# Kernel tuning notes

Hardware: AMD Instinct MI355X
Metric: run time of the kernel (lower is better)

Reference implementation:

```python
import jax, jax.numpy as jnp
import numpy as np

N_NODES = 50000
N_EDGES = 1600000
D_IN = 512
D_HEAD = 64
N_HEADS_L1 = 4


def _segment_mean(data, seg_ids, num_segments, counts):
    s = jax.ops.segment_sum(data, seg_ids, num_segments=num_segments)
    denom = jnp.maximum(counts, 1.0)
    return jnp.where(counts[:, None] > 0, s / denom[:, None], 0.0)


def setup_inputs() -> dict:
    key = jax.random.key(0)
    k1, k2, k3, k4 = jax.random.split(key, 4)
    node_features = jax.random.normal(k1, (N_NODES, D_IN), dtype=jnp.float32)
    edge_index = jax.random.randint(k2, (2, N_EDGES), 0, N_NODES, dtype=jnp.int32)
    W1 = jax.random.normal(k3, (N_HEADS_L1, D_IN, D_HEAD), dtype=jnp.float32) * (1.0 / np.sqrt(D_IN))
    W2 = jax.random.normal(k4, (N_HEADS_L1 * D_HEAD, D_HEAD), dtype=jnp.float32) * (1.0 / np.sqrt(N_HEADS_L1 * D_HEAD))
    return {"node_features": node_features, "edge_index": edge_index, "W1": W1, "W2": W2}


def reference(node_features, edge_index, W1, W2):
    n = node_features.shape[0]
    src = edge_index[0]  # segment ids (destination of aggregation in TF code)
    dst = edge_index[1]  # gathered neighbors
    counts = jax.ops.segment_sum(jnp.ones_like(src, dtype=node_features.dtype), src, num_segments=n)

    # Layer 1: 4 heads, Dense(64, no bias) -> gather(dst) -> unsorted_segment_mean(src) -> concat -> elu
    head_outs = []
    for i in range(N_HEADS_L1):
        t = node_features @ W1[i]                 # (N, 64)
        agg = _segment_mean(t[dst], src, n, counts)  # (N, 64)
        head_outs.append(agg)
    h = jax.nn.elu(jnp.concatenate(head_outs, axis=-1))  # (N, 256)

    # Layer 2: 1 head, linear activation
    t2 = h @ W2                                   # (N, 64)
    out = _segment_mean(t2[dst], src, n, counts)  # (N, 64)
    return out
```

## Files before the change

kernel.cpp:

```cpp
#include <hip/hip_runtime.h>
#include <hip/hip_bf16.h>
#include <stdint.h>

#define N_NODES 50000
#define N_EDGES 1600000
#define D_IN    512
#define D_H1    256
#define D_OUT   64

#define NBUK    196
#define MAXB    9216
#define EPB     4096
#define NPB     391
#define SLOT    96

typedef __attribute__((ext_vector_type(8))) short  short8;
typedef __attribute__((ext_vector_type(4))) float  f32x4;
typedef __attribute__((ext_vector_type(4))) unsigned int u32x4;
typedef __attribute__((ext_vector_type(2))) unsigned int u32x2;

static __device__ __forceinline__ unsigned short f2bf(float f) {
    union { float f; unsigned int u; } c; c.f = f;
    unsigned int u = c.u;
    return (unsigned short)((u + 0x7FFFu + ((u >> 16) & 1u)) >> 16);
}
static __device__ __forceinline__ float bf2f(unsigned short b) {
    union { unsigned int u; float f; } c; c.u = ((unsigned int)b) << 16;
    return c.f;
}
static __device__ __forceinline__ float bflo(unsigned int v) { return bf2f((unsigned short)(v & 0xffffu)); }
static __device__ __forceinline__ float bfhi(unsigned int v) { return bf2f((unsigned short)(v >> 16)); }


__global__ __launch_bounds__(256) void part_kernel(const int* __restrict__ src,
                                                   const int* __restrict__ dst,
                                                   int* __restrict__ gcnt,
                                                   unsigned int* __restrict__ gbuk) {
    __shared__ int hist[NBUK];
    __shared__ int lofs[NBUK];
    __shared__ int gbase[NBUK];
    __shared__ int sbuf[256];
    __shared__ unsigned int sorted[EPB];
    __shared__ unsigned char bid[EPB];

    const int t  = threadIdx.x;
    const int e0 = blockIdx.x * EPB;
    int ec = N_EDGES - e0; if (ec > EPB) ec = EPB;

    for (int i = t; i < NBUK; i += 256) hist[i] = 0;
    __syncthreads();

    unsigned int rec[16];
    int bb[16], idx[16];
#pragma unroll
    for (int j = 0; j < 16; ++j) {
        int i = j * 256 + t;
        if (i < ec) {
            int s = src[e0 + i], d = dst[e0 + i];
            int b = s >> 8;
            rec[j] = ((unsigned int)(s & 255) << 16) | (unsigned int)d;
            bb[j]  = b;
            idx[j] = atomicAdd(&hist[b], 1);
        } else bb[j] = -1;
    }
    __syncthreads();

    int v = (t < NBUK) ? hist[t] : 0;
    sbuf[t] = v;
    __syncthreads();
#pragma unroll
    for (int off = 1; off < 256; off <<= 1) {
        int x = (t >= off) ? sbuf[t - off] : 0;
        __syncthreads();
        sbuf[t] += x;
        __syncthreads();
    }
    if (t < NBUK) {
        lofs[t]  = sbuf[t] - v;
        gbase[t] = atomicAdd(&gcnt[t], v);
    }
    __syncthreads();

#pragma unroll
    for (int j = 0; j < 16; ++j) {
        if (bb[j] >= 0) {
            int p = lofs[bb[j]] + idx[j];
            sorted[p] = rec[j];
            bid[p] = (unsigned char)bb[j];
        }
    }
    __syncthreads();

    for (int i = t; i < ec; i += 256) {
        int b = bid[i];
        int p = gbase[b] + (i - lofs[b]);
        gbuk[(size_t)b * MAXB + p] = sorted[i];
    }
}


__global__ __launch_bounds__(256) void sort_kernel(const int* __restrict__ gcnt,
                                                   const unsigned int* __restrict__ gbuk,
                                                   unsigned short* __restrict__ sdst,
                                                   int* __restrict__ deg) {
    __shared__ int hist[256];
    __shared__ int nofs[256];
    __shared__ int sbuf[256];
    __shared__ unsigned short list[MAXB];

    const int t = threadIdx.x;
    const int b = blockIdx.x;
    const int cnt = gcnt[b];
    const unsigned int* buk = gbuk + (size_t)b * MAXB;

    hist[t] = 0;
    __syncthreads();
    for (int i = t; i < cnt; i += 256)
        atomicAdd(&hist[buk[i] >> 16], 1);
    __syncthreads();

    int v = hist[t];
    sbuf[t] = v;
    __syncthreads();
#pragma unroll
    for (int off = 1; off < 256; off <<= 1) {
        int x = (t >= off) ? sbuf[t - off] : 0;
        __syncthreads();
        sbuf[t] += x;
        __syncthreads();
    }
    nofs[t] = sbuf[t] - v;
    const int n = b * 256 + t;
    if (n < N_NODES) deg[n] = v;
    __syncthreads();

    for (int i = t; i < cnt; i += 256) {
        unsigned int r = buk[i];
        int p = atomicAdd(&nofs[r >> 16], 1);
        list[p] = (unsigned short)(r & 0xffffu);
    }
    __syncthreads();

    if (n < N_NODES && v > 0) {
        int beg = nofs[t] - v;
        unsigned short* out = sdst + (size_t)n * SLOT;
        for (int j = 0; j < v; ++j) out[j] = list[beg + j];
    }
}


__global__ void convw_kernel(const float* __restrict__ W1, const float* __restrict__ W2,
                             unsigned short* __restrict__ Bt1, unsigned short* __restrict__ Bt2) {
    int i = blockIdx.x * 256 + threadIdx.x;
    if (i < 4 * 512 * 64) {
        int h = i >> 15;
        int k = (i >> 6) & 511;
        int j = i & 63;
        Bt1[(h * 64 + j) * 512 + k] = f2bf(W1[i]);
    } else {
        int r = i - 4 * 512 * 64;
        if (r < 256 * 64) {
            int k = r >> 6;
            int n = r & 63;
            Bt2[n * 256 + k] = f2bf(W2[r]);
        }
    }
}


__global__ __launch_bounds__(512) void gemm1_kernel(const float* __restrict__ A,
                                                    const unsigned short* __restrict__ Bt,
                                                    unsigned short* __restrict__ C) {
    constexpr int BM = 128, BN = 256, BK = 32, LDK = 40, K = D_IN, M = N_NODES, N = D_H1;
    __shared__ unsigned short As[BM * LDK];
    __shared__ unsigned short Bs[BN * LDK];

    const int tid  = threadIdx.x;
    const int lane = tid & 63;
    const int w    = tid >> 6;
    const int wm   = (w >> 2) * 64;
    const int wn   = (w & 3) * 64;
    const int quad = lane >> 4;
    const int l15  = lane & 15;
    const int bm   = blockIdx.x;

    f32x4 acc[4][4];
#pragma unroll
    for (int mi = 0; mi < 4; ++mi)
#pragma unroll
        for (int ni = 0; ni < 4; ++ni)
            acc[mi][ni] = (f32x4){0.f, 0.f, 0.f, 0.f};

    const int r0 = tid >> 2;
    const int f8 = tid & 3;

    for (int k0 = 0; k0 < K; k0 += BK) {
        {
            int grow = bm * BM + r0;
            if (grow >= M) grow = M - 1;
            const float* ap = A + (size_t)grow * K + k0 + f8 * 8;
            f32x4 v0 = *(const f32x4*)ap;
            f32x4 v1 = *(const f32x4*)(ap + 4);
            u32x4 pk;
            pk[0] = (unsigned int)f2bf(v0[0]) | ((unsigned int)f2bf(v0[1]) << 16);
            pk[1] = (unsigned int)f2bf(v0[2]) | ((unsigned int)f2bf(v0[3]) << 16);
            pk[2] = (unsigned int)f2bf(v1[0]) | ((unsigned int)f2bf(v1[1]) << 16);
            pk[3] = (unsigned int)f2bf(v1[2]) | ((unsigned int)f2bf(v1[3]) << 16);
            *(u32x4*)&As[r0 * LDK + f8 * 8] = pk;
        }
        {
#pragma unroll
            for (int p = 0; p < 2; ++p) {
                int row = p * 128 + r0;
                u32x4 v = *(const u32x4*)(Bt + (size_t)row * K + k0 + f8 * 8);
                *(u32x4*)&Bs[row * LDK + f8 * 8] = v;
            }
        }
        __syncthreads();

        short8 af[4], bfr[4];
#pragma unroll
        for (int mi = 0; mi < 4; ++mi)
            af[mi] = *(const short8*)&As[(wm + mi * 16 + l15) * LDK + quad * 8];
#pragma unroll
        for (int ni = 0; ni < 4; ++ni)
            bfr[ni] = *(const short8*)&Bs[(wn + ni * 16 + l15) * LDK + quad * 8];
#pragma unroll
        for (int mi = 0; mi < 4; ++mi)
#pragma unroll
            for (int ni = 0; ni < 4; ++ni)
                acc[mi][ni] = __builtin_amdgcn_mfma_f32_16x16x32_bf16(af[mi], bfr[ni], acc[mi][ni], 0, 0, 0);
        __syncthreads();
    }

#pragma unroll
    for (int mi = 0; mi < 4; ++mi) {
        int row0 = bm * BM + wm + mi * 16 + quad * 4;
#pragma unroll
        for (int ni = 0; ni < 4; ++ni) {
            int col = wn + ni * 16 + l15;
#pragma unroll
            for (int r = 0; r < 4; ++r) {
                int row = row0 + r;
                if (row < M) C[(size_t)row * N + col] = f2bf(acc[mi][ni][r]);
            }
        }
    }
}


__global__ __launch_bounds__(256) void gemm2_kernel(const unsigned short* __restrict__ A,
                                                    const unsigned short* __restrict__ Bt,
                                                    unsigned short* __restrict__ C) {
    constexpr int BM = 64, BN = 64, BK = 32, LDK = 40, K = D_H1, M = N_NODES, N = D_OUT;
    __shared__ unsigned short As[BM * LDK];
    __shared__ unsigned short Bs[BN * LDK];

    const int tid  = threadIdx.x;
    const int lane = tid & 63;
    const int w    = tid >> 6;
    const int wm   = (w >> 1) * 32;
    const int wn   = (w & 1) * 32;
    const int quad = lane >> 4;
    const int l15  = lane & 15;
    const int bm   = blockIdx.x;

    f32x4 acc[2][2];
#pragma unroll
    for (int mi = 0; mi < 2; ++mi)
#pragma unroll
        for (int ni = 0; ni < 2; ++ni)
            acc[mi][ni] = (f32x4){0.f, 0.f, 0.f, 0.f};

    for (int k0 = 0; k0 < K; k0 += BK) {
        {
            int f8 = tid & 3;
            int r0 = tid >> 2;
            int grow = bm * BM + r0;
            if (grow >= M) grow = M - 1;
            u32x4 v = *(const u32x4*)(A + (size_t)grow * K + k0 + f8 * 8);
            *(u32x4*)&As[r0 * LDK + f8 * 8] = v;
        }
        {
            int f8 = tid & 3;
            int r0 = tid >> 2;
            u32x4 v = *(const u32x4*)(Bt + (size_t)r0 * K + k0 + f8 * 8);
            *(u32x4*)&Bs[r0 * LDK + f8 * 8] = v;
        }
        __syncthreads();

        short8 af[2], bfr[2];
#pragma unroll
        for (int mi = 0; mi < 2; ++mi)
            af[mi] = *(const short8*)&As[(wm + mi * 16 + l15) * LDK + quad * 8];
#pragma unroll
        for (int ni = 0; ni < 2; ++ni)
            bfr[ni] = *(const short8*)&Bs[(wn + ni * 16 + l15) * LDK + quad * 8];
#pragma unroll
        for (int mi = 0; mi < 2; ++mi)
#pragma unroll
            for (int ni = 0; ni < 2; ++ni)
                acc[mi][ni] = __builtin_amdgcn_mfma_f32_16x16x32_bf16(af[mi], bfr[ni], acc[mi][ni], 0, 0, 0);
        __syncthreads();
    }

#pragma unroll
    for (int mi = 0; mi < 2; ++mi) {
        int row0 = bm * BM + wm + mi * 16 + quad * 4;
#pragma unroll
        for (int ni = 0; ni < 2; ++ni) {
            int col = wn + ni * 16 + l15;
#pragma unroll
            for (int r = 0; r < 4; ++r) {
                int row = row0 + r;
                if (row < M) C[(size_t)row * N + col] = f2bf(acc[mi][ni][r]);
            }
        }
    }
}


__global__ __launch_bounds__(256) void agg1_kernel(const unsigned short* __restrict__ t,
                                                   const int* __restrict__ deg,
                                                   const unsigned short* __restrict__ sdst,
                                                   unsigned short* __restrict__ h) {
    int s = __builtin_amdgcn_readfirstlane(blockIdx.x * 4 + (threadIdx.x >> 6));
    int lane = threadIdx.x & 63;
    int sub = lane >> 5;
    int c   = lane & 31;
    int end = deg[s];
    const unsigned short* el = sdst + (size_t)s * SLOT;
    const unsigned short* base = t + 8 * c;

    float a[8];
#pragma unroll
    for (int k = 0; k < 8; ++k) a[k] = 0.f;

    int e = 0;
    for (; e + 8 <= end; e += 8) {
        int i0 = el[e + 0 + sub], i1 = el[e + 2 + sub];
        int i2 = el[e + 4 + sub], i3 = el[e + 6 + sub];
        u32x4 v0 = *(const u32x4*)(base + (size_t)i0 * D_H1);
        u32x4 v1 = *(const u32x4*)(base + (size_t)i1 * D_H1);
        u32x4 v2 = *(const u32x4*)(base + (size_t)i2 * D_H1);
        u32x4 v3 = *(const u32x4*)(base + (size_t)i3 * D_H1);
#pragma unroll
        for (int q = 0; q < 4; ++q) {
            a[2 * q]     += (bflo(v0[q]) + bflo(v1[q])) + (bflo(v2[q]) + bflo(v3[q]));
            a[2 * q + 1] += (bfhi(v0[q]) + bfhi(v1[q])) + (bfhi(v2[q]) + bfhi(v3[q]));
        }
    }
    for (; e + 2 <= end; e += 2) {
        int i0 = el[e + sub];
        u32x4 v = *(const u32x4*)(base + (size_t)i0 * D_H1);
#pragma unroll
        for (int q = 0; q < 4; ++q) {
            a[2 * q]     += bflo(v[q]);
            a[2 * q + 1] += bfhi(v[q]);
        }
    }
    if (e < end && sub == 0) {
        int i0 = el[e];
        u32x4 v = *(const u32x4*)(base + (size_t)i0 * D_H1);
#pragma unroll
        for (int q = 0; q < 4; ++q) {
            a[2 * q]     += bflo(v[q]);
            a[2 * q + 1] += bfhi(v[q]);
        }
    }
#pragma unroll
    for (int k = 0; k < 8; ++k) a[k] += __shfl_xor(a[k], 32);

    if (sub == 0) {
        float iv = (end > 0) ? (1.0f / (float)end) : 0.f;
        u32x4 pk;
#pragma unroll
        for (int q = 0; q < 4; ++q) {
            float m0 = a[2 * q] * iv, m1 = a[2 * q + 1] * iv;
            m0 = (m0 > 0.f) ? m0 : (__expf(m0) - 1.f);
            m1 = (m1 > 0.f) ? m1 : (__expf(m1) - 1.f);
            pk[q] = (unsigned int)f2bf(m0) | ((unsigned int)f2bf(m1) << 16);
        }
        *(u32x4*)&h[(size_t)s * D_H1 + 8 * c] = pk;
    }
}

__global__ __launch_bounds__(256) void agg2_kernel(const unsigned short* __restrict__ t2,
                                                   const int* __restrict__ deg,
                                                   const unsigned short* __restrict__ sdst,
                                                   float* __restrict__ out) {
    int s = __builtin_amdgcn_readfirstlane(blockIdx.x * 4 + (threadIdx.x >> 6));
    int lane = threadIdx.x & 63;
    int sub = lane >> 4;
    int c   = lane & 15;
    int end = deg[s];
    const unsigned short* el = sdst + (size_t)s * SLOT;
    const unsigned short* bb = t2 + 4 * c;

    float a0 = 0.f, a1 = 0.f, a2 = 0.f, a3 = 0.f;
    int e = 0;
    for (; e + 8 <= end; e += 8) {
        int i0 = el[e + sub], i1 = el[e + 4 + sub];
        u32x2 v0 = *(const u32x2*)(bb + (size_t)i0 * D_OUT);
        u32x2 v1 = *(const u32x2*)(bb + (size_t)i1 * D_OUT);
        a0 += bflo(v0[0]) + bflo(v1[0]);
        a1 += bfhi(v0[0]) + bfhi(v1[0]);
        a2 += bflo(v0[1]) + bflo(v1[1]);
        a3 += bfhi(v0[1]) + bfhi(v1[1]);
    }
    for (; e + 4 <= end; e += 4) {
        int i0 = el[e + sub];
        u32x2 v = *(const u32x2*)(bb + (size_t)i0 * D_OUT);
        a0 += bflo(v[0]); a1 += bfhi(v[0]); a2 += bflo(v[1]); a3 += bfhi(v[1]);
    }
    int rem = end - e;
    if (sub < rem) {
        int i0 = el[e + sub];
        u32x2 v = *(const u32x2*)(bb + (size_t)i0 * D_OUT);
        a0 += bflo(v[0]); a1 += bfhi(v[0]); a2 += bflo(v[1]); a3 += bfhi(v[1]);
    }
    a0 += __shfl_xor(a0, 16); a1 += __shfl_xor(a1, 16);
    a2 += __shfl_xor(a2, 16); a3 += __shfl_xor(a3, 16);
    a0 += __shfl_xor(a0, 32); a1 += __shfl_xor(a1, 32);
    a2 += __shfl_xor(a2, 32); a3 += __shfl_xor(a3, 32);
    if (sub == 0) {
        float iv = (end > 0) ? (1.0f / (float)end) : 0.f;
        f32x4 r; r[0] = a0 * iv; r[1] = a1 * iv; r[2] = a2 * iv; r[3] = a3 * iv;
        *(f32x4*)(out + (size_t)s * D_OUT + 4 * c) = r;
    }
}


extern "C" void kernel_launch(void* const* d_in, const int* in_sizes, int n_in,
                              void* d_out, int out_size, void* d_ws, size_t ws_size,
                              hipStream_t stream) {
    const float* X  = (const float*)d_in[0];
    const int*   ei = (const int*)d_in[1];
    const float* W1 = (const float*)d_in[2];
    const float* W2 = (const float*)d_in[3];
    const int* src = ei;
    const int* dst = ei + N_EDGES;

    char* ws = (char*)d_ws;
    size_t off = 0;
    auto alloc = [&](size_t bytes) {
        off = (off + 255) & ~(size_t)255;
        void* p = ws + off;
        off += bytes;
        return p;
    };
    int*          gcnt = (int*)alloc((size_t)NBUK * 4);
    unsigned int* gbuk = (unsigned int*)alloc((size_t)NBUK * MAXB * 4);
    unsigned short* sdst = (unsigned short*)alloc(((size_t)N_NODES * SLOT + 64) * 2);
    int*          deg  = (int*)alloc((size_t)N_NODES * 4);
    unsigned short* Bt1 = (unsigned short*)alloc((size_t)D_H1 * D_IN * 2);
    unsigned short* Bt2 = (unsigned short*)alloc((size_t)D_OUT * D_H1 * 2);
    unsigned short* t1  = (unsigned short*)alloc((size_t)N_NODES * D_H1 * 2);
    unsigned short* h   = (unsigned short*)alloc((size_t)N_NODES * D_H1 * 2);
    unsigned short* t2  = (unsigned short*)alloc((size_t)N_NODES * D_OUT * 2);

    hipMemsetAsync(gcnt, 0, (size_t)NBUK * 4, stream);

    part_kernel<<<NPB, 256, 0, stream>>>(src, dst, gcnt, gbuk);
    sort_kernel<<<NBUK, 256, 0, stream>>>(gcnt, gbuk, sdst, deg);
    convw_kernel<<<(4 * 512 * 64 + 256 * 64 + 255) / 256, 256, 0, stream>>>(W1, W2, Bt1, Bt2);

    gemm1_kernel<<<(N_NODES + 127) / 128, 512, 0, stream>>>(X, Bt1, t1);
    agg1_kernel<<<N_NODES / 4, 256, 0, stream>>>(t1, deg, sdst, h);
    gemm2_kernel<<<(N_NODES + 63) / 64, 256, 0, stream>>>(h, Bt2, t2);
    agg2_kernel<<<N_NODES / 4, 256, 0, stream>>>(t2, deg, sdst, (float*)d_out);
}
```

Baseline: 360.1 us.

## Store GEMM outputs in column-sliced layout and split aggregation by feature slice

```diff
diff --git a/kernel.cpp b/kernel.cpp
--- a/kernel.cpp
+++ b/kernel.cpp
@@ -161,6 +161,13 @@
         int r = i - 4 * 512 * 64;
         if (r < 256 * 64) {
             int k = r >> 6;
+            int n = r & 6 * 10 + 3;
+        }
+    }
+    if (i >= 4 * 512 * 64) {
+        int r = i - 4 * 512 * 64;
+        if (r < 256 * 64) {
+            int k = r >> 6;
             int n = r & 63;
             Bt2[n * 256 + k] = f2bf(W2[r]);
         }
@@ -171,9 +178,9 @@
 __global__ __launch_bounds__(512) void gemm1_kernel(const float* __restrict__ A,
                                                     const unsigned short* __restrict__ Bt,
                                                     unsigned short* __restrict__ C) {
-    constexpr int BM = 128, BN = 256, BK = 32, LDK = 40, K = D_IN, M = N_NODES, N = D_H1;
+    constexpr int BM = 128, BK = 32, LDK = 40, K = D_IN, M = N_NODES;
     __shared__ unsigned short As[BM * LDK];
-    __shared__ unsigned short Bs[BN * LDK];
+    __shared__ unsigned short Bs[256 * LDK];
 
     const int tid  = threadIdx.x;
     const int lane = tid & 63;
@@ -239,10 +246,11 @@
 #pragma unroll
         for (int ni = 0; ni < 4; ++ni) {
             int col = wn + ni * 16 + l15;
+            unsigned short* cp = C + (size_t)(col >> 5) * ((size_t)N_NODES * 32) + (col & 31);
 #pragma unroll
             for (int r = 0; r < 4; ++r) {
                 int row = row0 + r;
-                if (row < M) C[(size_t)row * N + col] = f2bf(acc[mi][ni][r]);
+                if (row < M) cp[(size_t)row * 32] = f2bf(acc[mi][ni][r]);
             }
         }
     }
@@ -252,9 +260,9 @@
 __global__ __launch_bounds__(256) void gemm2_kernel(const unsigned short* __restrict__ A,
                                                     const unsigned short* __restrict__ Bt,
                                                     unsigned short* __restrict__ C) {
-    constexpr int BM = 64, BN = 64, BK = 32, LDK = 40, K = D_H1, M = N_NODES, N = D_OUT;
+    constexpr int BM = 64, BK = 32, LDK = 40, K = D_H1, M = N_NODES;
     __shared__ unsigned short As[BM * LDK];
-    __shared__ unsigned short Bs[BN * LDK];
+    __shared__ unsigned short Bs[64 * LDK];
 
     const int tid  = threadIdx.x;
     const int lane = tid & 63;
@@ -310,10 +318,11 @@
 #pragma unroll
         for (int ni = 0; ni < 2; ++ni) {
             int col = wn + ni * 16 + l15;
+            unsigned short* cp = C + (size_t)(col >> 5) * ((size_t)N_NODES * 32) + (col & 31);
 #pragma unroll
             for (int r = 0; r < 4; ++r) {
                 int row = row0 + r;
-                if (row < M) C[(size_t)row * N + col] = f2bf(acc[mi][ni][r]);
+                if (row < M) cp[(size_t)row * 32] = f2bf(acc[mi][ni][r]);
             }
         }
     }
@@ -324,109 +333,91 @@
                                                    const int* __restrict__ deg,
                                                    const unsigned short* __restrict__ sdst,
                                                    unsigned short* __restrict__ h) {
-    int s = __builtin_amdgcn_readfirstlane(blockIdx.x * 4 + (threadIdx.x >> 6));
-    int lane = threadIdx.x & 63;
-    int sub = lane >> 5;
-    int c   = lane & 31;
-    int end = deg[s];
+    const int bi    = blockIdx.x;
+    const int slice = bi & 7;
+    const int s     = __builtin_amdgcn_readfirstlane((bi >> 3) * 4 + (threadIdx.x >> 6));
+    const int lane  = threadIdx.x & 63;
+    const int sub   = lane >> 3;
+    const int cc    = lane & 7;
+    const int end   = __builtin_nontemporal_load(deg + s);
     const unsigned short* el = sdst + (size_t)s * SLOT;
-    const unsigned short* base = t + 8 * c;
-
-    float a[8];
-#pragma unroll
-    for (int k = 0; k < 8; ++k) a[k] = 0.f;
-
-    int e = 0;
-    for (; e + 8 <= end; e += 8) {
-        int i0 = el[e + 0 + sub], i1 = el[e + 2 + sub];
-        int i2 = el[e + 4 + sub], i3 = el[e + 6 + sub];
-        u32x4 v0 = *(const u32x4*)(base + (size_t)i0 * D_H1);
-        u32x4 v1 = *(const u32x4*)(base + (size_t)i1 * D_H1);
-        u32x4 v2 = *(const u32x4*)(base + (size_t)i2 * D_H1);
-        u32x4 v3 = *(const u32x4*)(base + (size_t)i3 * D_H1);
-#pragma unroll
-        for (int q = 0; q < 4; ++q) {
-            a[2 * q]     += (bflo(v0[q]) + bflo(v1[q])) + (bflo(v2[q]) + bflo(v3[q]));
-            a[2 * q + 1] += (bfhi(v0[q]) + bfhi(v1[q])) + (bfhi(v2[q]) + bfhi(v3[q]));
-        }
-    }
-    for (; e + 2 <= end; e += 2) {
-        int i0 = el[e + sub];
-        u32x4 v = *(const u32x4*)(base + (size_t)i0 * D_H1);
-#pragma unroll
-        for (int q = 0; q < 4; ++q) {
-            a[2 * q]     += bflo(v[q]);
-            a[2 * q + 1] += bfhi(v[q]);
-        }
-    }
-    if (e < end && sub == 0) {
-        int i0 = el[e];
-        u32x4 v = *(const u32x4*)(base + (size_t)i0 * D_H1);
-#pragma unroll
-        for (int q = 0; q < 4; ++q) {
-            a[2 * q]     += bflo(v[q]);
-            a[2 * q + 1] += bfhi(v[q]);
-        }
-    }
-#pragma unroll
-    for (int k = 0; k < 8; ++k) a[k] += __shfl_xor(a[k], 32);
+    const int elv   = __builtin_nontemporal_load(el + lane);
+    const unsigned short* base = t + (size_t)slice * ((size_t)N_NODES * 32) + cc * 4;
+
+    float a0 = 0.f, a1 = 0.f, a2 = 0.f, a3 = 0.f;
+    for (int e = 0; e < end; e += 16) {
+        int s0 = e + sub, s1 = e + 8 + sub;
+        int i0 = __shfl(elv, s0 & 63);
+        int i1 = __shfl(elv, s1 & 63);
+        if (s0 >= 64) i0 = el[s0];
+        if (s1 >= 64) i1 = el[s1];
+        if (s0 < end) {
+            u32x2 v = *(const u32x2*)(base + ((unsigned)i0 << 5));
+            a0 += bflo(v[0]); a1 += bfhi(v[0]); a2 += bflo(v[1]); a3 += bfhi(v[1]);
+        }
+        if (s1 < end) {
+            u32x2 v = *(const u32x2*)(base + ((unsigned)i1 << 5));
+            a0 += bflo(v[0]); a1 += bfhi(v[0]); a2 += bflo(v[1]); a3 += bfhi(v[1]);
+        }
+    }
+    a0 += __shfl_xor(a0, 8);  a1 += __shfl_xor(a1, 8);  a2 += __shfl_xor(a2, 8);  a3 += __shfl_xor(a3, 8);
+    a0 += __shfl_xor(a0, 16); a1 += __shfl_xor(a1, 16); a2 += __shfl_xor(a2, 16); a3 += __shfl_xor(a3, 16);
+    a0 += __shfl_xor(a0, 32); a1 += __shfl_xor(a1, 32); a2 += __shfl_xor(a2, 32); a3 += __shfl_xor(a3, 32);
 
     if (sub == 0) {
         float iv = (end > 0) ? (1.0f / (float)end) : 0.f;
-        u32x4 pk;
-#pragma unroll
-        for (int q = 0; q < 4; ++q) {
-            float m0 = a[2 * q] * iv, m1 = a[2 * q + 1] * iv;
-            m0 = (m0 > 0.f) ? m0 : (__expf(m0) - 1.f);
-            m1 = (m1 > 0.f) ? m1 : (__expf(m1) - 1.f);
-            pk[q] = (unsigned int)f2bf(m0) | ((unsigned int)f2bf(m1) << 16);
-        }
-        *(u32x4*)&h[(size_t)s * D_H1 + 8 * c] = pk;
-    }
-}
+        float m0 = a0 * iv, m1 = a1 * iv, m2 = a2 * iv, m3 = a3 * iv;
+        m0 = (m0 > 0.f) ? m0 : (__expf(m0) - 1.f);
+        m1 = (m1 > 0.f) ? m1 : (__expf(m1) - 1.f);
+        m2 = (m2 > 0.f) ? m2 : (__expf(m2) - 1.f);
+        m3 = (m3 > 0.f) ? m3 : (__expf(m3) - 1.f);
+        u32x2 pk;
+        pk[0] = (unsigned int)f2bf(m0) | ((unsigned int)f2bf(m1) << 16);
+        pk[1] = (unsigned int)f2bf(m2) | ((unsigned int)f2bf(m3) << 16);
+        *(u32x2*)&h[(size_t)s * D_H1 + slice * 32 + cc * 4] = pk;
+    }
+}
+
 
 __global__ __launch_bounds__(256) void agg2_kernel(const unsigned short* __restrict__ t2,
                                                    const int* __restrict__ deg,
                                                    const unsigned short* __restrict__ sdst,
                                                    float* __restrict__ out) {
-    int s = __builtin_amdgcn_readfirstlane(blockIdx.x * 4 + (threadIdx.x >> 6));
-    int lane = threadIdx.x & 63;
-    int sub = lane >> 4;
-    int c   = lane & 15;
-    int end = deg[s];
+    const int bi    = blockIdx.x;
+    const int slice = bi & 1;
+    const int s     = __builtin_amdgcn_readfirstlane((bi >> 1) * 4 + (threadIdx.x >> 6));
+    const int lane  = threadIdx.x & 63;
+    const int sub   = lane >> 3;
+    const int cc    = lane & 7;
+    const int end   = __builtin_nontemporal_load(deg + s);
     const unsigned short* el = sdst + (size_t)s * SLOT;
-    const unsigned short* bb = t2 + 4 * c;
+    const int elv   = __builtin_nontemporal_load(el + lane);
+    const unsigned short* base = t2 + (size_t)slice * ((size_t)N_NODES * 32) + cc * 4;
 
     float a0 = 0.f, a1 = 0.f, a2 = 0.f, a3 = 0.f;
-    int e = 0;
-    for (; e + 8 <= end; e += 8) {
-        int i0 = el[e + sub], i1 = el[e + 4 + sub];
-        u32x2 v0 = *(const u32x2*)(bb + (size_t)i0 * D_OUT);
-        u32x2 v1 = *(const u32x2*)(bb + (size_t)i1 * D_OUT);
-        a0 += bflo(v0[0]) + bflo(v1[0]);
-        a1 += bfhi(v0[0]) + bfhi(v1[0]);
-        a2 += bflo(v0[1]) + bflo(v1[1]);
-        a3 += bfhi(v0[1]) + bfhi(v1[1]);
-    }
-    for (; e + 4 <= end; e += 4) {
-        int i0 = el[e + sub];
-        u32x2 v = *(const u32x2*)(bb + (size_t)i0 * D_OUT);
-        a0 += bflo(v[0]); a1 += bfhi(v[0]); a2 += bflo(v[1]); a3 += bfhi(v[1]);
-    }
-    int rem = end - e;
-    if (sub < rem) {
-        int i0 = el[e + sub];
-        u32x2 v = *(const u32x2*)(bb + (size_t)i0 * D_OUT);
-        a0 += bflo(v[0]); a1 += bfhi(v[0]); a2 += bflo(v[1]); a3 += bfhi(v[1]);
-    }
-    a0 += __shfl_xor(a0, 16); a1 += __shfl_xor(a1, 16);
-    a2 += __shfl_xor(a2, 16); a3 += __shfl_xor(a3, 16);
-    a0 += __shfl_xor(a0, 32); a1 += __shfl_xor(a1, 32);
-    a2 += __shfl_xor(a2, 32); a3 += __shfl_xor(a3, 32);
+    for (int e = 0; e < end; e += 16) {
+        int s0 = e + sub, s1 = e + 8 + sub;
+        int i0 = __shfl(elv, s0 & 63);
+        int i1 = __shfl(elv, s1 & 63);
+        if (s0 >= 64) i0 = el[s0];
+        if (s1 >= 64) i1 = el[s1];
+        if (s0 < end) {
+            u32x2 v = *(const u32x2*)(base + ((unsigned)i0 << 5));
+            a0 += bflo(v[0]); a1 += bfhi(v[0]); a2 += bflo(v[1]); a3 += bfhi(v[1]);
+        }
+        if (s1 < end) {
+            u32x2 v = *(const u32x2*)(base + ((unsigned)i1 << 5));
+            a0 += bflo(v[0]); a1 += bfhi(v[0]); a2 += bflo(v[1]); a3 += bfhi(v[1]);
+        }
+    }
+    a0 += __shfl_xor(a0, 8);  a1 += __shfl_xor(a1, 8);  a2 += __shfl_xor(a2, 8);  a3 += __shfl_xor(a3, 8);
+    a0 += __shfl_xor(a0, 16); a1 += __shfl_xor(a1, 16); a2 += __shfl_xor(a2, 16); a3 += __shfl_xor(a3, 16);
+    a0 += __shfl_xor(a0, 32); a1 += __shfl_xor(a1, 32); a2 += __shfl_xor(a2, 32); a3 += __shfl_xor(a3, 32);
+
     if (sub == 0) {
         float iv = (end > 0) ? (1.0f / (float)end) : 0.f;
         f32x4 r; r[0] = a0 * iv; r[1] = a1 * iv; r[2] = a2 * iv; r[3] = a3 * iv;
-        *(f32x4*)(out + (size_t)s * D_OUT + 4 * c) = r;
+        *(f32x4*)(out + (size_t)s * D_OUT + slice * 32 + cc * 4) = r;
     }
 }
 
@@ -466,7 +457,7 @@
     convw_kernel<<<(4 * 512 * 64 + 256 * 64 + 255) / 256, 256, 0, stream>>>(W1, W2, Bt1, Bt2);
 
     gemm1_kernel<<<(N_NODES + 127) / 128, 512, 0, stream>>>(X, Bt1, t1);
-    agg1_kernel<<<N_NODES / 4, 256, 0, stream>>>(t1, deg, sdst, h);
+    agg1_kernel<<<(N_NODES / 4) * 8, 256, 0, stream>>>(t1, deg, sdst, h);
     gemm2_kernel<<<(N_NODES + 63) / 64, 256, 0, stream>>>(h, Bt2, t2);
-    agg2_kernel<<<N_NODES / 4, 256, 0, stream>>>(t2, deg, sdst, (float*)d_out);
-}
+    agg2_kernel<<<(N_NODES / 4) * 2, 256, 0, stream>>>(t2, deg, sdst, (float*)d_out);
+}
```

After: 423.2 us. 17.5% more time.
